# Optimization experiments

Hardware: AMD Instinct MI355X
Metric: run time of the kernel (lower is better)

Reference implementation:

```python
import jax, jax.numpy as jnp
import numpy as np

ANGSTROM2BOHR = 1.8897261258369282
CUTOFF_ANGSTROM = 5.2  # module's `cutoff` init arg, converted to bohr in forward


def smooth_cutoff(d, rc):
    # torchani 'smooth' cutoff: exp(1 - 1/(1 - (d/rc)^2)) for d < rc, else 0
    x2 = (d / rc) ** 2
    x2_safe = jnp.where(x2 < 1.0, x2, 0.0)  # avoid inf inside the masked branch
    return jnp.where(d < rc, jnp.exp(1.0 - 1.0 / (1.0 - x2_safe)), 0.0)


def setup_inputs() -> dict:
    key = jax.random.key(0)
    k0, k1, k2, k3 = jax.random.split(key, 4)
    n_mol, n_atoms, n_pairs = 4096, 64, 16 * 1024 * 1024
    n_elem = 4  # H, C, N, O
    species = jax.random.randint(k0, (n_mol, n_atoms), 0, n_elem)
    energies = jnp.zeros((n_mol,), jnp.float32)
    atom_index12 = jax.random.randint(k1, (2, n_pairs), 0, n_mol * n_atoms)
    distances = jax.random.uniform(k2, (n_pairs,), jnp.float32, 0.5, 6.0)  # angstrom
    # exp_prefactor = -scaling_charge * sqrt(outer(Z, Z)) / 2, Z = [1, 6, 7, 8]
    z = jnp.array([1.0, 6.0, 7.0, 8.0], jnp.float32)
    exp_prefactor = (-0.016 * jnp.sqrt(jnp.outer(z, z)) / 2.0).astype(jnp.float32)
    # distances_factor = -scaling_radius / cutoff_radii (symmetric pairwise radii table)
    radii = jax.random.uniform(k3, (n_elem, n_elem), jnp.float32, 2.0, 5.0)
    radii = 0.5 * (radii + radii.T)
    distances_factor = (-10.0 / radii).astype(jnp.float32)
    return {
        "species": species,
        "energies": energies,
        "atom_index12": atom_index12,
        "distances": distances,
        "exp_prefactor": exp_prefactor,
        "distances_factor": distances_factor,
    }


def reference(species, energies, atom_index12, distances, exp_prefactor, distances_factor):
    n_mol, n_atoms = species.shape
    d = distances * ANGSTROM2BOHR  # [P]
    species12 = species.reshape(-1)[atom_index12]  # [2, P] gather
    pre = exp_prefactor[species12[0], species12[1]]   # [P]
    dfac = distances_factor[species12[0], species12[1]]  # [P]
    srb = pre * jnp.exp(dfac * d)
    srb = srb * smooth_cutoff(d, CUTOFF_ANGSTROM * ANGSTROM2BOHR)
    mol_idx = atom_index12[0] // n_atoms  # [P]
    out = energies + jax.ops.segment_sum(srb, mol_idx, num_segments=n_mol)
    return species, out
```

## Files before the change

kernel.cpp:

```cpp
#include <hip/hip_runtime.h>
#include <math.h>


#define NT        1024
#define NBLK      256
#define SCALE_F   134217728.0f
#define INV_SCALE 7.450580596923828125e-9

__global__ void pack_species_kernel(const int* __restrict__ sp,
                                    unsigned* __restrict__ packed, int nwords) {
    int w = blockIdx.x * blockDim.x + threadIdx.x;
    if (w >= nwords) return;
    const int4* p4 = (const int4*)(sp + (w << 4));
    int4 a = p4[0], b = p4[1], c = p4[2], d = p4[3];
    unsigned v =
        (unsigned)(a.x & 3)        | ((unsigned)(a.y & 3) << 2)  |
        ((unsigned)(a.z & 3) << 4) | ((unsigned)(a.w & 3) << 6)  |
        ((unsigned)(b.x & 3) << 8) | ((unsigned)(b.y & 3) << 10) |
        ((unsigned)(b.z & 3) << 12)| ((unsigned)(b.w & 3) << 14) |
        ((unsigned)(c.x & 3) << 16)| ((unsigned)(c.y & 3) << 18) |
        ((unsigned)(c.z & 3) << 20)| ((unsigned)(c.w & 3) << 22) |
        ((unsigned)(d.x & 3) << 24)| ((unsigned)(d.y & 3) << 26) |
        ((unsigned)(d.z & 3) << 28)| ((unsigned)(d.w & 3) << 30);
    packed[w] = v;
}

__global__ void init_kernel(const int* __restrict__ species,
                            float* __restrict__ out,
                            unsigned long long* __restrict__ acc,
                            int n_species, int n_mol) {
    int i = blockIdx.x * blockDim.x + threadIdx.x;
    if (i < n_species) out[i] = (float)species[i];
    if (i < n_mol)     acc[i] = 0ull;
}

__global__ __launch_bounds__(NT, 1)
void srb_fused_u32(const unsigned* __restrict__ packed_ws,
                   const int* __restrict__ ai,
                   const float* __restrict__ dist,
                   const float* __restrict__ pre_tab,
                   const float* __restrict__ dfac_tab,
                   unsigned long long* __restrict__ acc,
                   int P, int mol_shift) {
    __shared__ unsigned packed[16384];
    __shared__ unsigned binsu[4096];
    __shared__ float2 tabr[4][18];

    const int t = threadIdx.x;
    for (int i = t; i < 4096; i += NT) binsu[i] = 0u;
    if (t < 64) {
        int e = t & 15;
        tabr[t >> 4][e] = make_float2(-pre_tab[e], dfac_tab[e]);
    }
    {
        int4* dst = (int4*)packed;
        const int4* src = (const int4*)packed_ws;
        for (int i = t; i < 4096; i += NT) dst[i] = src[i];
    }
    __syncthreads();

    const float a2b   = (float)1.8897261258369282;
    const float rc    = (float)(5.2 * 1.8897261258369282);
    const float rcinv = (float)(1.0 / (5.2 * 1.8897261258369282));
    const int   copy  = t & 3;

    const int ng     = P >> 3;
    const int stride = (int)gridDim.x * NT;
    const int4*   v0 = (const int4*)ai;
    const int4*   v1 = (const int4*)(ai + P);
    const float4* dv = (const float4*)dist;

    for (int g = (int)blockIdx.x * NT + t; g < ng; g += stride) {
        int4   i0a = v0[2 * g], i0b = v0[2 * g + 1];
        int4   i1a = v1[2 * g], i1b = v1[2 * g + 1];
        float4 da  = dv[2 * g], db4 = dv[2 * g + 1];

        unsigned a0[8] = { (unsigned)i0a.x, (unsigned)i0a.y, (unsigned)i0a.z,
                           (unsigned)i0a.w, (unsigned)i0b.x, (unsigned)i0b.y,
                           (unsigned)i0b.z, (unsigned)i0b.w };
        unsigned a1[8] = { (unsigned)i1a.x, (unsigned)i1a.y, (unsigned)i1a.z,
                           (unsigned)i1a.w, (unsigned)i1b.x, (unsigned)i1b.y,
                           (unsigned)i1b.z, (unsigned)i1b.w };
        float    dd[8] = { da.x, da.y, da.z, da.w, db4.x, db4.y, db4.z, db4.w };

        unsigned w0[8], w1[8];
        #pragma unroll
        for (int k = 0; k < 8; ++k) w0[k] = packed[a0[k] >> 4];
        #pragma unroll
        for (int k = 0; k < 8; ++k) w1[k] = packed[a1[k] >> 4];

        float2 td[8];
        #pragma unroll
        for (int k = 0; k < 8; ++k) {
            unsigned s0 = (w0[k] >> ((a0[k] & 15u) << 1)) & 3u;
            unsigned s1 = (w1[k] >> ((a1[k] & 15u) << 1)) & 3u;
            td[k] = tabr[copy][(s0 << 2) | s1];
        }

        unsigned q[8];
        #pragma unroll
        for (int k = 0; k < 8; ++k) {
            float db  = dd[k] * a2b;
            float x   = db * rcinv;
            float arg = td[k].y * db + (1.0f - 1.0f / (1.0f - x * x));
            float mag = td[k].x * __expf(arg);
            mag = (db < rc) ? mag : 0.0f;
            q[k] = (unsigned)(mag * SCALE_F);
        }

        #pragma unroll
        for (int k = 0; k < 8; ++k)
            atomicAdd(&binsu[a0[k] >> mol_shift], q[k]);
    }

    __syncthreads();
    for (int i = t; i < 4096; i += NT) {
        unsigned v = binsu[i];
        if (v) atomicAdd(&acc[i], (unsigned long long)v);
    }
}

__global__ void final_kernel(const unsigned long long* __restrict__ acc,
                             const float* __restrict__ energies,
                             float* __restrict__ out_e, int n_mol) {
    int m = blockIdx.x * blockDim.x + threadIdx.x;
    if (m < n_mol)
        out_e[m] = energies[m] - (float)((double)acc[m] * INV_SCALE);
}

__global__ void init_out_fallback(const int* __restrict__ species,
                                  const float* __restrict__ energies,
                                  float* __restrict__ out,
                                  int n_species, int n_mol) {
    int i = blockIdx.x * blockDim.x + threadIdx.x;
    if (i < n_species) out[i] = (float)species[i];
    else if (i < n_species + n_mol) out[i] = energies[i - n_species];
}

__global__ __launch_bounds__(NT, 1)
void srb_fused_f32(const int* __restrict__ species,
                   const int* __restrict__ ai,
                   const float* __restrict__ dist,
                   const float* __restrict__ pre_tab,
                   const float* __restrict__ dfac_tab,
                   float* __restrict__ out_e,
                   int P, int mol_shift) {
    __shared__ unsigned packed[16384];
    __shared__ float bins[4096];
    __shared__ float2 tab[16];
    const int t = threadIdx.x;
    for (int i = t; i < 4096; i += NT) bins[i] = 0.0f;
    if (t < 16) tab[t] = make_float2(pre_tab[t], dfac_tab[t]);
    for (int w = t; w < 16384; w += NT) {
        const int4* p4 = (const int4*)(species + (w << 4));
        int4 a = p4[0], b = p4[1], c = p4[2], d = p4[3];
        unsigned v =
            (unsigned)(a.x & 3)        | ((unsigned)(a.y & 3) << 2)  |
            ((unsigned)(a.z & 3) << 4) | ((unsigned)(a.w & 3) << 6)  |
            ((unsigned)(b.x & 3) << 8) | ((unsigned)(b.y & 3) << 10) |
            ((unsigned)(b.z & 3) << 12)| ((unsigned)(b.w & 3) << 14) |
            ((unsigned)(c.x & 3) << 16)| ((unsigned)(c.y & 3) << 18) |
            ((unsigned)(c.z & 3) << 20)| ((unsigned)(c.w & 3) << 22) |
            ((unsigned)(d.x & 3) << 24)| ((unsigned)(d.y & 3) << 26) |
            ((unsigned)(d.z & 3) << 28)| ((unsigned)(d.w & 3) << 30);
        packed[w] = v;
    }
    __syncthreads();
    const float a2b   = (float)1.8897261258369282;
    const float rc    = (float)(5.2 * 1.8897261258369282);
    const float rcinv = (float)(1.0 / (5.2 * 1.8897261258369282));
    auto body = [&](int a0, int a1, float dang) {
        unsigned ua0 = (unsigned)a0, ua1 = (unsigned)a1;
        unsigned s0 = (packed[ua0 >> 4] >> ((ua0 & 15u) << 1)) & 3u;
        unsigned s1 = (packed[ua1 >> 4] >> ((ua1 & 15u) << 1)) & 3u;
        float2 td = tab[(s0 << 2) | s1];
        float db = dang * a2b;
        float x  = db * rcinv;
        float arg = td.y * db + (1.0f - 1.0f / (1.0f - x * x));
        float srb = td.x * __expf(arg);
        srb = (db < rc) ? srb : 0.0f;
        atomicAdd(&bins[ua0 >> mol_shift], srb);
    };
    const int nv = P >> 2, stride = (int)gridDim.x * NT;
    const int4* v0 = (const int4*)ai;
    const int4* v1 = (const int4*)(ai + P);
    const float4* dv = (const float4*)dist;
    for (int v = (int)blockIdx.x * NT + t; v < nv; v += stride) {
        int4 i0 = v0[v]; int4 i1 = v1[v]; float4 dd = dv[v];
        body(i0.x, i1.x, dd.x); body(i0.y, i1.y, dd.y);
        body(i0.z, i1.z, dd.z); body(i0.w, i1.w, dd.w);
    }
    __syncthreads();
    for (int i = t; i < 4096; i += NT) {
        float s = bins[i];
        if (s != 0.0f) atomicAdd(&out_e[i], s);
    }
}

extern "C" void kernel_launch(void* const* d_in, const int* in_sizes, int n_in,
                              void* d_out, int out_size, void* d_ws, size_t ws_size,
                              hipStream_t stream) {
    const int*   species  = (const int*)d_in[0];
    const float* energies = (const float*)d_in[1];
    const int*   ai       = (const int*)d_in[2];
    const float* dist     = (const float*)d_in[3];
    const float* pre_tab  = (const float*)d_in[4];
    const float* dfac_tab = (const float*)d_in[5];

    const int n_species = in_sizes[0];
    const int n_mol     = in_sizes[1];
    const int P         = in_sizes[3];
    const int n_atoms   = n_species / n_mol;

    int mol_shift = 0;
    while ((1 << mol_shift) < n_atoms) ++mol_shift;

    float* out   = (float*)d_out;
    float* out_e = out + n_species;

    const int    nwords    = n_species / 16;
    const size_t packed_sz = (size_t)nwords * 4;
    const size_t acc_sz    = (size_t)n_mol * 8;
    const size_t need      = packed_sz + acc_sz;

    if (ws_size >= need && (P & 7) == 0) {
        unsigned*           packed = (unsigned*)d_ws;
        unsigned long long* acc    = (unsigned long long*)((char*)d_ws + packed_sz);

        init_kernel<<<(n_species + 255) / 256, 256, 0, stream>>>(
            species, out, acc, n_species, n_mol);
        pack_species_kernel<<<(nwords + 255) / 256, 256, 0, stream>>>(
            species, packed, nwords);
        srb_fused_u32<<<NBLK, NT, 0, stream>>>(
            packed, ai, dist, pre_tab, dfac_tab, acc, P, mol_shift);
        final_kernel<<<(n_mol + 255) / 256, 256, 0, stream>>>(
            acc, energies, out_e, n_mol);
    } else {
        init_out_fallback<<<(n_species + n_mol + 255) / 256, 256, 0, stream>>>(
            species, energies, out, n_species, n_mol);
        srb_fused_f32<<<NBLK, NT, 0, stream>>>(
            species, ai, dist, pre_tab, dfac_tab, out_e, P, mol_shift);
    }
}
```

Before: 250.6 us.

## Stage pair streams into LDS with async global_load_lds per contiguous block chunk

Adds a new main kernel that gives each block a contiguous slice of pairs and streams the index and distance arrays into LDS chunks using the global_load_lds builtin, then has each thread read four pairs from LDS. The aim is to bypass register round-trips for the streamed inputs and get more coalesced bulk loads. The staging is not double-buffered, so every chunk waits on a barrier before compute. The f32 fallback path is removed and the u32 fallback is simplified to scalar loads.

```diff
diff --git a/kernel.cpp b/kernel.cpp
--- a/kernel.cpp
+++ b/kernel.cpp
@@ -4,8 +4,16 @@
 
 #define NT        1024
 #define NBLK      256
+#define CSTAGE    4096
 #define SCALE_F   134217728.0f
 #define INV_SCALE 7.450580596923828125e-9
+
+typedef const __attribute__((address_space(1))) unsigned gas_u32;
+typedef __attribute__((address_space(3))) unsigned       las_u32;
+
+__device__ __forceinline__ void stage16(const void* g, void* l) {
+    __builtin_amdgcn_global_load_lds((gas_u32*)g, (las_u32*)l, 16, 0, 0);
+}
 
 __global__ void pack_species_kernel(const int* __restrict__ sp,
                                     unsigned* __restrict__ packed, int nwords) {
@@ -34,6 +42,109 @@
     if (i < n_mol)     acc[i] = 0ull;
 }
 
+__global__ __launch_bounds__(NT, 4)
+void srb_async(const unsigned* __restrict__ packed_ws,
+               const int* __restrict__ ai,
+               const float* __restrict__ dist,
+               const float* __restrict__ pre_tab,
+               const float* __restrict__ dfac_tab,
+               unsigned long long* __restrict__ acc,
+               int P, int mol_shift) {
+    __shared__ unsigned packed[16384];
+    __shared__ unsigned binsu[4096];
+    __shared__ unsigned sa0[CSTAGE];
+    __shared__ unsigned sa1[CSTAGE];
+    __shared__ float    sd [CSTAGE];
+    __shared__ float2   tabr[4][18];
+
+    const int t = threadIdx.x;
+    for (int i = t; i < 4096; i += NT) binsu[i] = 0u;
+    if (t < 64) {
+        int e = t & 15;
+        tabr[t >> 4][e] = make_float2(-pre_tab[e], dfac_tab[e]);
+    }
+    {
+        int4* dst = (int4*)packed;
+        const int4* src = (const int4*)packed_ws;
+        for (int i = t; i < 4096; i += NT) dst[i] = src[i];
+    }
+
+    const float a2b   = (float)1.8897261258369282;
+    const float rc    = (float)(5.2 * 1.8897261258369282);
+    const float rcinv = (float)(1.0 / (5.2 * 1.8897261258369282));
+    const int   copy  = t & 3;
+    const int   wave  = t >> 6;
+    const int   lane  = t & 63;
+
+    const unsigned* ai0 = (const unsigned*)ai;
+    const unsigned* ai1 = (const unsigned*)(ai + P);
+
+    const int ppb  = P / (int)gridDim.x;
+    const int base = (int)blockIdx.x * ppb;
+
+    const int woff = wave << 8;
+    unsigned* lds0 = &sa0[woff];
+    unsigned* lds1 = &sa1[woff];
+    float*    ldsd = &sd[woff];
+
+    __syncthreads();
+
+    for (int s = 0; s < ppb; s += CSTAGE) {
+        const int goff = base + s + woff + (lane << 2);
+        stage16(ai0  + goff, lds0);
+        stage16(ai1  + goff, lds1);
+        stage16(dist + goff, ldsd);
+        __syncthreads();
+
+        uint4  A0 = ((const uint4*)sa0)[t];
+        uint4  A1 = ((const uint4*)sa1)[t];
+        float4 DD = ((const float4*)sd)[t];
+
+        unsigned a0[4] = { A0.x, A0.y, A0.z, A0.w };
+        unsigned a1[4] = { A1.x, A1.y, A1.z, A1.w };
+        float    dd[4] = { DD.x, DD.y, DD.z, DD.w };
+
+        unsigned w0[4], w1[4];
+        #pragma unroll
+        for (int k = 0; k < 4; ++k) w0[k] = packed[a0[k] >> 4];
+        #pragma unroll
+        for (int k = 0; k < 4; ++k) w1[k] = packed[a1[k] >> 4];
+
+        float2 td[4];
+        #pragma unroll
+        for (int k = 0; k < 4; ++k) {
+            unsigned s0 = (w0[k] >> ((a0[k] & 15u) << 1)) & 3u;
+            unsigned s1 = (w1[k] >> ((a1[k] & 15u) << 1)) & 3u;
+            td[k] = tabr[copy][(s0 << 2) | s1];
+        }
+
+        #pragma unroll
+        for (int k = 0; k < 4; ++k) {
+            float db  = dd[k] * a2b;
+            float x   = db * rcinv;
+            float arg = td[k].y * db + (1.0f - 1.0f / (1.0f - x * x));
+            float mag = td[k].x * __expf(arg);
+            mag = (db < rc) ? mag : 0.0f;
+            unsigned q = (unsigned)(mag * SCALE_F);
+            atomicAdd(&binsu[a0[k] >> mol_shift], q);
+        }
+        __syncthreads();
+    }
+
+    for (int i = t; i < 4096; i += NT) {
+        unsigned v = binsu[i];
+        if (v) atomicAdd(&acc[i], (unsigned long long)v);
+    }
+}
+
+__global__ void final_kernel(const unsigned long long* __restrict__ acc,
+                             const float* __restrict__ energies,
+                             float* __restrict__ out_e, int n_mol) {
+    int m = blockIdx.x * blockDim.x + threadIdx.x;
+    if (m < n_mol)
+        out_e[m] = energies[m] - (float)((double)acc[m] * INV_SCALE);
+}
+
 __global__ __launch_bounds__(NT, 1)
 void srb_fused_u32(const unsigned* __restrict__ packed_ws,
                    const int* __restrict__ ai,
@@ -45,7 +156,6 @@
     __shared__ unsigned packed[16384];
     __shared__ unsigned binsu[4096];
     __shared__ float2 tabr[4][18];
-
     const int t = threadIdx.x;
     for (int i = t; i < 4096; i += NT) binsu[i] = 0u;
     if (t < 64) {
@@ -58,142 +168,29 @@
         for (int i = t; i < 4096; i += NT) dst[i] = src[i];
     }
     __syncthreads();
-
     const float a2b   = (float)1.8897261258369282;
     const float rc    = (float)(5.2 * 1.8897261258369282);
     const float rcinv = (float)(1.0 / (5.2 * 1.8897261258369282));
     const int   copy  = t & 3;
-
-    const int ng     = P >> 3;
+    auto body = [&](unsigned ua0, unsigned ua1, float dang) {
+        unsigned s0 = (packed[ua0 >> 4] >> ((ua0 & 15u) << 1)) & 3u;
+        unsigned s1 = (packed[ua1 >> 4] >> ((ua1 & 15u) << 1)) & 3u;
+        float2 td = tabr[copy][(s0 << 2) | s1];
+        float db = dang * a2b;
+        float x  = db * rcinv;
+        float arg = td.y * db + (1.0f - 1.0f / (1.0f - x * x));
+        float mag = td.x * __expf(arg);
+        mag = (db < rc) ? mag : 0.0f;
+        unsigned q = (unsigned)(mag * SCALE_F);
+        atomicAdd(&binsu[ua0 >> mol_shift], q);
+    };
     const int stride = (int)gridDim.x * NT;
-    const int4*   v0 = (const int4*)ai;
-    const int4*   v1 = (const int4*)(ai + P);
-    const float4* dv = (const float4*)dist;
-
-    for (int g = (int)blockIdx.x * NT + t; g < ng; g += stride) {
-        int4   i0a = v0[2 * g], i0b = v0[2 * g + 1];
-        int4   i1a = v1[2 * g], i1b = v1[2 * g + 1];
-        float4 da  = dv[2 * g], db4 = dv[2 * g + 1];
-
-        unsigned a0[8] = { (unsigned)i0a.x, (unsigned)i0a.y, (unsigned)i0a.z,
-                           (unsigned)i0a.w, (unsigned)i0b.x, (unsigned)i0b.y,
-                           (unsigned)i0b.z, (unsigned)i0b.w };
-        unsigned a1[8] = { (unsigned)i1a.x, (unsigned)i1a.y, (unsigned)i1a.z,
-                           (unsigned)i1a.w, (unsigned)i1b.x, (unsigned)i1b.y,
-                           (unsigned)i1b.z, (unsigned)i1b.w };
-        float    dd[8] = { da.x, da.y, da.z, da.w, db4.x, db4.y, db4.z, db4.w };
-
-        unsigned w0[8], w1[8];
-        #pragma unroll
-        for (int k = 0; k < 8; ++k) w0[k] = packed[a0[k] >> 4];
-        #pragma unroll
-        for (int k = 0; k < 8; ++k) w1[k] = packed[a1[k] >> 4];
-
-        float2 td[8];
-        #pragma unroll
-        for (int k = 0; k < 8; ++k) {
-            unsigned s0 = (w0[k] >> ((a0[k] & 15u) << 1)) & 3u;
-            unsigned s1 = (w1[k] >> ((a1[k] & 15u) << 1)) & 3u;
-            td[k] = tabr[copy][(s0 << 2) | s1];
-        }
-
-        unsigned q[8];
-        #pragma unroll
-        for (int k = 0; k < 8; ++k) {
-            float db  = dd[k] * a2b;
-            float x   = db * rcinv;
-            float arg = td[k].y * db + (1.0f - 1.0f / (1.0f - x * x));
-            float mag = td[k].x * __expf(arg);
-            mag = (db < rc) ? mag : 0.0f;
-            q[k] = (unsigned)(mag * SCALE_F);
-        }
-
-        #pragma unroll
-        for (int k = 0; k < 8; ++k)
-            atomicAdd(&binsu[a0[k] >> mol_shift], q[k]);
-    }
-
+    for (int p = (int)blockIdx.x * NT + t; p < P; p += stride)
+        body((unsigned)ai[p], (unsigned)ai[P + p], dist[p]);
     __syncthreads();
     for (int i = t; i < 4096; i += NT) {
         unsigned v = binsu[i];
         if (v) atomicAdd(&acc[i], (unsigned long long)v);
-    }
-}
-
-__global__ void final_kernel(const unsigned long long* __restrict__ acc,
-                             const float* __restrict__ energies,
-                             float* __restrict__ out_e, int n_mol) {
-    int m = blockIdx.x * blockDim.x + threadIdx.x;
-    if (m < n_mol)
-        out_e[m] = energies[m] - (float)((double)acc[m] * INV_SCALE);
-}
-
-__global__ void init_out_fallback(const int* __restrict__ species,
-                                  const float* __restrict__ energies,
-                                  float* __restrict__ out,
-                                  int n_species, int n_mol) {
-    int i = blockIdx.x * blockDim.x + threadIdx.x;
-    if (i < n_species) out[i] = (float)species[i];
-    else if (i < n_species + n_mol) out[i] = energies[i - n_species];
-}
-
-__global__ __launch_bounds__(NT, 1)
-void srb_fused_f32(const int* __restrict__ species,
-                   const int* __restrict__ ai,
-                   const float* __restrict__ dist,
-                   const float* __restrict__ pre_tab,
-                   const float* __restrict__ dfac_tab,
-                   float* __restrict__ out_e,
-                   int P, int mol_shift) {
-    __shared__ unsigned packed[16384];
-    __shared__ float bins[4096];
-    __shared__ float2 tab[16];
-    const int t = threadIdx.x;
-    for (int i = t; i < 4096; i += NT) bins[i] = 0.0f;
-    if (t < 16) tab[t] = make_float2(pre_tab[t], dfac_tab[t]);
-    for (int w = t; w < 16384; w += NT) {
-        const int4* p4 = (const int4*)(species + (w << 4));
-        int4 a = p4[0], b = p4[1], c = p4[2], d = p4[3];
-        unsigned v =
-            (unsigned)(a.x & 3)        | ((unsigned)(a.y & 3) << 2)  |
-            ((unsigned)(a.z & 3) << 4) | ((unsigned)(a.w & 3) << 6)  |
-            ((unsigned)(b.x & 3) << 8) | ((unsigned)(b.y & 3) << 10) |
-            ((unsigned)(b.z & 3) << 12)| ((unsigned)(b.w & 3) << 14) |
-            ((unsigned)(c.x & 3) << 16)| ((unsigned)(c.y & 3) << 18) |
-            ((unsigned)(c.z & 3) << 20)| ((unsigned)(c.w & 3) << 22) |
-            ((unsigned)(d.x & 3) << 24)| ((unsigned)(d.y & 3) << 26) |
-            ((unsigned)(d.z & 3) << 28)| ((unsigned)(d.w & 3) << 30);
-        packed[w] = v;
-    }
-    __syncthreads();
-    const float a2b   = (float)1.8897261258369282;
-    const float rc    = (float)(5.2 * 1.8897261258369282);
-    const float rcinv = (float)(1.0 / (5.2 * 1.8897261258369282));
-    auto body = [&](int a0, int a1, float dang) {
-        unsigned ua0 = (unsigned)a0, ua1 = (unsigned)a1;
-        unsigned s0 = (packed[ua0 >> 4] >> ((ua0 & 15u) << 1)) & 3u;
-        unsigned s1 = (packed[ua1 >> 4] >> ((ua1 & 15u) << 1)) & 3u;
-        float2 td = tab[(s0 << 2) | s1];
-        float db = dang * a2b;
-        float x  = db * rcinv;
-        float arg = td.y * db + (1.0f - 1.0f / (1.0f - x * x));
-        float srb = td.x * __expf(arg);
-        srb = (db < rc) ? srb : 0.0f;
-        atomicAdd(&bins[ua0 >> mol_shift], srb);
-    };
-    const int nv = P >> 2, stride = (int)gridDim.x * NT;
-    const int4* v0 = (const int4*)ai;
-    const int4* v1 = (const int4*)(ai + P);
-    const float4* dv = (const float4*)dist;
-    for (int v = (int)blockIdx.x * NT + t; v < nv; v += stride) {
-        int4 i0 = v0[v]; int4 i1 = v1[v]; float4 dd = dv[v];
-        body(i0.x, i1.x, dd.x); body(i0.y, i1.y, dd.y);
-        body(i0.z, i1.z, dd.z); body(i0.w, i1.w, dd.w);
-    }
-    __syncthreads();
-    for (int i = t; i < 4096; i += NT) {
-        float s = bins[i];
-        if (s != 0.0f) atomicAdd(&out_e[i], s);
     }
 }
 
@@ -221,24 +218,23 @@
     const int    nwords    = n_species / 16;
     const size_t packed_sz = (size_t)nwords * 4;
     const size_t acc_sz    = (size_t)n_mol * 8;
-    const size_t need      = packed_sz + acc_sz;
-
-    if (ws_size >= need && (P & 7) == 0) {
-        unsigned*           packed = (unsigned*)d_ws;
-        unsigned long long* acc    = (unsigned long long*)((char*)d_ws + packed_sz);
-
-        init_kernel<<<(n_species + 255) / 256, 256, 0, stream>>>(
-            species, out, acc, n_species, n_mol);
-        pack_species_kernel<<<(nwords + 255) / 256, 256, 0, stream>>>(
-            species, packed, nwords);
+
+    unsigned*           packed = (unsigned*)d_ws;
+    unsigned long long* acc    = (unsigned long long*)((char*)d_ws + packed_sz);
+    (void)acc_sz;
+
+    init_kernel<<<(n_species + 255) / 256, 256, 0, stream>>>(
+        species, out, acc, n_species, n_mol);
+    pack_species_kernel<<<(nwords + 255) / 256, 256, 0, stream>>>(
+        species, packed, nwords);
+
+    if ((P % (NBLK * CSTAGE)) == 0) {
+        srb_async<<<NBLK, NT, 0, stream>>>(
+            packed, ai, dist, pre_tab, dfac_tab, acc, P, mol_shift);
+    } else {
         srb_fused_u32<<<NBLK, NT, 0, stream>>>(
             packed, ai, dist, pre_tab, dfac_tab, acc, P, mol_shift);
-        final_kernel<<<(n_mol + 255) / 256, 256, 0, stream>>>(
-            acc, energies, out_e, n_mol);
-    } else {
-        init_out_fallback<<<(n_species + n_mol + 255) / 256, 256, 0, stream>>>(
-            species, energies, out, n_species, n_mol);
-        srb_fused_f32<<<NBLK, NT, 0, stream>>>(
-            species, ai, dist, pre_tab, dfac_tab, out_e, P, mol_shift);
-    }
-}
+    }
+    final_kernel<<<(n_mol + 255) / 256, 256, 0, stream>>>(
+        acc, energies, out_e, n_mol);
+}
```

New measurement: 250.7 us. No clear change (+0.0%).
